# Optimization experiments

Measured on AMD Instinct MI355X. Metric: run time of the kernel, lower is better.

## Reference

```python
import jax, jax.numpy as jnp
import numpy as np

B, T, D = 2, 4096, 512
H = 8
HS = D // H  # 64
CTX = 4096


def setup_inputs() -> dict:
    key = jax.random.key(0)
    ks = jax.random.split(key, 10)
    s = lambda fan_in: fan_in ** -0.5
    x = jax.random.normal(ks[0], (B, T, D), dtype=jnp.float32)
    # per-head q/k/v projections (no bias), stacked over heads: [H, D, HS]
    Wq = jax.random.normal(ks[1], (H, D, HS), dtype=jnp.float32) * s(D)
    Wk = jax.random.normal(ks[2], (H, D, HS), dtype=jnp.float32) * s(D)
    Wv = jax.random.normal(ks[3], (H, D, HS), dtype=jnp.float32) * s(D)
    # output projection [D, D] + bias
    Wproj = jax.random.normal(ks[4], (D, D), dtype=jnp.float32) * s(D)
    bproj = jax.random.normal(ks[5], (D,), dtype=jnp.float32) * 0.01
    # feed-forward: D -> 4D -> D
    W1 = jax.random.normal(ks[6], (D, 4 * D), dtype=jnp.float32) * s(D)
    b1 = jax.random.normal(ks[7], (4 * D,), dtype=jnp.float32) * 0.01
    W2 = jax.random.normal(ks[8], (4 * D, D), dtype=jnp.float32) * s(4 * D)
    b2 = jax.random.normal(ks[9], (D,), dtype=jnp.float32) * 0.01
    return {"x": x, "Wq": Wq, "Wk": Wk, "Wv": Wv, "Wproj": Wproj,
            "bproj": bproj, "W1": W1, "b1": b1, "W2": W2, "b2": b2}


def reference(x, Wq, Wk, Wv, Wproj, bproj, W1, b1, W2, b2):
    Bx, Tx, Dx = x.shape
    scale = HS ** -0.5
    # multi-head causal self-attention (naive, full TxT scores as in source)
    q = jnp.einsum('btd,hde->bhte', x, Wq)
    k = jnp.einsum('btd,hde->bhte', x, Wk)
    v = jnp.einsum('btd,hde->bhte', x, Wv)
    wei = jnp.einsum('bhte,bhse->bhts', q, k) * scale  # [B,H,T,T]
    causal = jnp.tril(jnp.ones((Tx, Tx), dtype=bool))
    wei = jnp.where(causal, wei, -jnp.inf)
    wei = jax.nn.softmax(wei, axis=-1)
    attn = jnp.einsum('bhts,bhse->bhte', wei, v)  # [B,H,T,HS]
    # concat heads (cat along last dim == transpose+reshape of stacked heads)
    attn = attn.transpose(0, 2, 1, 3).reshape(Bx, Tx, Dx)
    sa_out = attn @ Wproj + bproj
    x = x + sa_out
    # feed-forward with residual
    h = jax.nn.relu(x @ W1 + b1)
    x = x + (h @ W2 + b2)
    return x
```

## Files before the change

### kernel.cpp

```cpp
#include <hip/hip_runtime.h>


typedef __attribute__((ext_vector_type(8))) short bf16x8;
typedef __attribute__((ext_vector_type(4))) float f32x4;
typedef __attribute__((ext_vector_type(16))) float f32x16;
typedef unsigned short u16;

__device__ __forceinline__ u16 f2bf(float f) {
  union { float f; unsigned int i; } u; u.f = f;
  unsigned int r = u.i + 0x7fffu + ((u.i >> 16) & 1u);
  return (u16)(r >> 16);
}
__device__ __forceinline__ float bf2f(u16 s) {
  union { unsigned int i; float f; } u; u.i = ((unsigned int)s) << 16;
  return u.f;
}
__device__ __forceinline__ void gload16(const void* g, void* l) {
  __builtin_amdgcn_global_load_lds((const __attribute__((address_space(1))) void*)g,
                                   (__attribute__((address_space(3))) void*)l,
                                   16, 0, 0);
}

__device__ __forceinline__ void plswap_u(unsigned &a, unsigned &b) {
#if defined(__has_builtin) && __has_builtin(__builtin_amdgcn_permlane32_swap)
  auto r = __builtin_amdgcn_permlane32_swap(a, b, false, false);
  a = (unsigned)r[0]; b = (unsigned)r[1];
#else
  asm("v_permlane32_swap_b32 %0, %1" : "+v"(a), "+v"(b));
#endif
}
__device__ __forceinline__ void plswap_f(float &a, float &b) {
  unsigned ua = __builtin_bit_cast(unsigned, a), ub = __builtin_bit_cast(unsigned, b);
  plswap_u(ua, ub);
  a = __builtin_bit_cast(float, ua); b = __builtin_bit_cast(float, ub);
}

__device__ __forceinline__ float tsum16(const f32x16 v) {
  float a = v[0] + v[8],  b = v[1] + v[9];
  float c = v[2] + v[10], d = v[3] + v[11];
  float e = v[4] + v[12], f = v[5] + v[13];
  float g = v[6] + v[14], h = v[7] + v[15];
  a += e; b += f; c += g; d += h;
  a += c; b += d;
  return a + b;
}

__global__ void cast_x_kernel(const float4* __restrict__ in, ushort4* __restrict__ out, int n4) {
  int i = blockIdx.x * blockDim.x + threadIdx.x;
  if (i >= n4) return;
  float4 v = in[i];
  ushort4 o; o.x = f2bf(v.x); o.y = f2bf(v.y); o.z = f2bf(v.z); o.w = f2bf(v.w);
  out[i] = o;
}

__global__ void transpose_cast_kernel(const float* __restrict__ in, u16* __restrict__ out,
                                      int C, int ldo, long in_z, long out_z) {
  __shared__ float t[32][33];
  in += (long)blockIdx.z * in_z;
  out += (long)blockIdx.z * out_z;
  int c0 = blockIdx.x * 32, r0 = blockIdx.y * 32;
  int tx = threadIdx.x & 31, ty = threadIdx.x >> 5;
#pragma unroll
  for (int k = 0; k < 4; k++)
    t[ty + 8 * k][tx] = in[(long)(r0 + ty + 8 * k) * C + c0 + tx];
  __syncthreads();
#pragma unroll
  for (int k = 0; k < 4; k++)
    out[(long)(c0 + ty + 8 * k) * ldo + r0 + tx] = f2bf(t[tx][ty + 8 * k]);
}

__global__ void transpose_v_kernel(const u16* __restrict__ qkv, u16* __restrict__ vt) {
  __shared__ u16 t[32][33];
  int z = blockIdx.z;
  const u16* in = qkv + (long)(z >> 3) * 4096 * 1536 + 1024 + (z & 7) * 64;
  u16* out = vt + (long)z * 64 * 4096;
  int c0 = blockIdx.x * 32, r0 = blockIdx.y * 32;
  int tx = threadIdx.x & 31, ty = threadIdx.x >> 5;
#pragma unroll
  for (int k = 0; k < 4; k++)
    t[ty + 8 * k][tx] = in[(long)(r0 + ty + 8 * k) * 1536 + c0 + tx];
  __syncthreads();
#pragma unroll
  for (int k = 0; k < 4; k++)
    out[(long)(c0 + ty + 8 * k) * 4096 + r0 + tx] = t[tx][ty + 8 * k];
}

template <int MODE, int BN>
__global__ __launch_bounds__(256) void gemm_bt_kernel(
    const u16* __restrict__ A, const u16* __restrict__ Bt, void* __restrict__ Out,
    const float* __restrict__ bias, const float* __restrict__ resf,
    const u16* __restrict__ resb, int N, int K) {
  __shared__ __align__(16) char As[128 * 128];
  __shared__ __align__(16) char Bs[BN * 128];
  const int tid = threadIdx.x;
  const int lane = tid & 63, w = tid >> 6;
  const int l15 = lane & 15, l4 = lane >> 4;
  const int nx = gridDim.x, nwg = nx * gridDim.y;
  int id = blockIdx.y * nx + blockIdx.x;
  id = (id & 7) * (nwg >> 3) + (id >> 3);
  const long m0 = (long)(id / nx) * 128;
  const long n0 = (long)(id % nx) * BN;
  const int wm = (w >> 1) * 64, wn = (w & 1) * (BN / 2);
  const int NB = BN / 32;

  f32x4 acc[4][NB] = {};

  for (int kt = 0; kt < K; kt += 64) {
#pragma unroll
    for (int i = 0; i < 4; i++) {
      int basechunk = i * 256 + w * 64;
      int chunk = basechunk + lane;
      int row = chunk >> 3, c = chunk & 7;
      int sc = c ^ (row & 7);
      gload16(A + (m0 + row) * K + kt + sc * 8, As + basechunk * 16);
    }
#pragma unroll
    for (int i = 0; i < BN / 32; i++) {
      int basechunk = i * 256 + w * 64;
      int chunk = basechunk + lane;
      int row = chunk >> 3, c = chunk & 7;
      int sc = c ^ (row & 7);
      gload16(Bt + (n0 + row) * K + kt + sc * 8, Bs + basechunk * 16);
    }
    __syncthreads();
#pragma unroll
    for (int kk = 0; kk < 2; kk++) {
      bf16x8 a[4], b[NB];
#pragma unroll
      for (int m = 0; m < 4; m++) {
        int row = wm + m * 16 + l15;
        int ch = (kk * 4 + l4) ^ (row & 7);
        a[m] = *(const bf16x8*)(As + row * 128 + ch * 16);
      }
#pragma unroll
      for (int n = 0; n < NB; n++) {
        int row = wn + n * 16 + l15;
        int ch = (kk * 4 + l4) ^ (row & 7);
        b[n] = *(const bf16x8*)(Bs + row * 128 + ch * 16);
      }
#pragma unroll
      for (int m = 0; m < 4; m++)
#pragma unroll
        for (int n = 0; n < NB; n++)
          acc[m][n] = __builtin_amdgcn_mfma_f32_16x16x32_bf16(a[m], b[n], acc[m][n], 0, 0, 0);
    }
    __syncthreads();
  }

#pragma unroll
  for (int m = 0; m < 4; m++) {
#pragma unroll
    for (int n = 0; n < NB; n++) {
      long gcol = n0 + wn + n * 16 + l15;
#pragma unroll
      for (int r = 0; r < 4; r++) {
        long grow = m0 + wm + m * 16 + l4 * 4 + r;
        float v = acc[m][n][r];
        if (MODE == 0) {
          ((u16*)Out)[grow * N + gcol] = f2bf(v);
        } else if (MODE == 1) {
          v += bias[gcol] + resf[grow * N + gcol];
          ((u16*)Out)[grow * N + gcol] = f2bf(v);
        } else if (MODE == 2) {
          v += bias[gcol];
          v = v > 0.f ? v : 0.f;
          ((u16*)Out)[grow * N + gcol] = f2bf(v);
        } else {
          v += bias[gcol] + bf2f(resb[grow * N + gcol]);
          ((float*)Out)[grow * N + gcol] = v;
        }
      }
    }
  }
}

__global__ __launch_bounds__(512, 4) void attn_kernel(
    const u16* __restrict__ qkv, const u16* __restrict__ vt,
    u16* __restrict__ pacc, float* __restrict__ pli) {
  __shared__ __align__(16) char Ks[2][64 * 128];
  __shared__ __align__(16) char Vs[2][64 * 128];
  const int tid = threadIdx.x;
  const int lane = tid & 63, w = tid >> 6;
  const int l31 = lane & 31, l5 = lane >> 5;
  const float cexp = 0.18033688f;

  const int g = blockIdx.x;

  for (int it = 0; it < 2; ++it) {
    const int item = it ? 1023 - g : g;
    const int qt = item >> 6;
    const int bh = (item >> 2) & 15;
    const int qq = item & 3;
    const int b = bh >> 3, h = bh & 7;
    const int qt0 = qt * 256;
    const int L = qt + 1;
    const int j0 = qq * L, j1 = j0 + L;
    const int jdiag = 4 * qt;
    const u16* qbase = qkv + (long)b * 4096 * 1536 + h * 64;
    const u16* kbase = qbase + 512;
    const u16* vtbase = vt + (long)bh * 64 * 4096;

    const int qrow_g = qt0 + w * 32 + l31;
    bf16x8 aq[4];
    {
      const u16* qp = qbase + (long)qrow_g * 1536 + l5 * 8;
#pragma unroll
      for (int kk = 0; kk < 4; kk++) aq[kk] = *(const bf16x8*)(qp + kk * 16);
    }

    {
      int row = tid >> 3, c = tid & 7, sc = c ^ (row & 7);
      gload16(kbase + (long)(j0 * 64 + row) * 1536 + sc * 8, Ks[0] + w * 1024);
      gload16(vtbase + (long)row * 4096 + j0 * 64 + sc * 8, Vs[0] + w * 1024);
    }
    __syncthreads();

    f32x16 oacc[2] = {};
    float li = 0.f;

    for (int j = j0; j < j1; ++j) {
      const int cur = (j - j0) & 1;
      if (j + 1 < j1) {
        int row = tid >> 3, c = tid & 7, sc = c ^ (row & 7);
        gload16(kbase + (long)((j + 1) * 64 + row) * 1536 + sc * 8, Ks[cur ^ 1] + w * 1024);
        gload16(vtbase + (long)row * 4096 + (j + 1) * 64 + sc * 8, Vs[cur ^ 1] + w * 1024);
      }

      const bool diag = (j >= jdiag);
      const int thr = qrow_g - j * 64;

#pragma unroll
      for (int n = 0; n < 2; n++) {
        f32x16 st = {};
        __builtin_amdgcn_s_setprio(1);
#pragma unroll
        for (int kk = 0; kk < 4; kk++) {
          int ch = ((l5 + 2 * kk) ^ (l31 & 7)) * 16;
          bf16x8 ak = *(const bf16x8*)(Ks[cur] + (n * 32 + l31) * 128 + ch);
          st = __builtin_amdgcn_mfma_f32_32x32x16_bf16(ak, aq[kk], st, 0, 0, 0);
        }
        __builtin_amdgcn_s_setprio(0);

        if (diag) {
#pragma unroll
          for (int reg = 0; reg < 16; reg++) {
            int key = n * 32 + 4 * l5 + (reg & 3) + 8 * (reg >> 2);
            if (key > thr) st[reg] = -1e30f;
          }
        }

#pragma unroll
        for (int reg = 0; reg < 16; reg++)
          st[reg] = exp2f(fmaf(st[reg], cexp, -12.f));
        li += tsum16(st);

#pragma unroll
        for (int jj = 0; jj < 2; jj++) {
          unsigned w0, w1, w2, w3;
          {
            unsigned pa, pb;
            asm("v_cvt_pk_bf16_f32 %0, %1, %2" : "=v"(pa) : "v"(st[(2 * jj) * 4 + 0]), "v"(st[(2 * jj) * 4 + 1]));
            asm("v_cvt_pk_bf16_f32 %0, %1, %2" : "=v"(pb) : "v"(st[(2 * jj + 1) * 4 + 0]), "v"(st[(2 * jj + 1) * 4 + 1]));
            plswap_u(pa, pb);
            w0 = pa; w2 = pb;
          }
          {
            unsigned pa, pb;
            asm("v_cvt_pk_bf16_f32 %0, %1, %2" : "=v"(pa) : "v"(st[(2 * jj) * 4 + 2]), "v"(st[(2 * jj) * 4 + 3]));
            asm("v_cvt_pk_bf16_f32 %0, %1, %2" : "=v"(pb) : "v"(st[(2 * jj + 1) * 4 + 2]), "v"(st[(2 * jj + 1) * 4 + 3]));
            plswap_u(pa, pb);
            w1 = pa; w3 = pb;
          }
          union { unsigned u[4]; bf16x8 v; } bp;
          bp.u[0] = w0; bp.u[1] = w1; bp.u[2] = w2; bp.u[3] = w3;
          int s = 2 * n + jj;
          int ch = ((l5 + 2 * s) ^ (l31 & 7)) * 16;
          bf16x8 av0 = *(const bf16x8*)(Vs[cur] + l31 * 128 + ch);
          bf16x8 av1 = *(const bf16x8*)(Vs[cur] + (32 + l31) * 128 + ch);
          __builtin_amdgcn_s_setprio(1);
          oacc[0] = __builtin_amdgcn_mfma_f32_32x32x16_bf16(av0, bp.v, oacc[0], 0, 0, 0);
          oacc[1] = __builtin_amdgcn_mfma_f32_32x32x16_bf16(av1, bp.v, oacc[1], 0, 0, 0);
          __builtin_amdgcn_s_setprio(0);
        }
      }
      __syncthreads();
    }

    {
      float ta = li, tb = li;
      plswap_f(ta, tb);
      li = ta + tb;
    }

    u16* pa = pacc + (long)item * 16384;
#pragma unroll
    for (int ne = 0; ne < 2; ne++)
#pragma unroll
      for (int gg = 0; gg < 4; gg++) {
        ushort4 o;
        o.x = f2bf(oacc[ne][4 * gg + 0]);
        o.y = f2bf(oacc[ne][4 * gg + 1]);
        o.z = f2bf(oacc[ne][4 * gg + 2]);
        o.w = f2bf(oacc[ne][4 * gg + 3]);
        *(ushort4*)(pa + (w * 32 + l31) * 64 + ne * 32 + 4 * l5 + 8 * gg) = o;
      }
    if (l5 == 0) pli[(long)item * 256 + w * 32 + l31] = li;
  }
}

__global__ __launch_bounds__(256) void attn_merge_kernel(
    const u16* __restrict__ pacc, const float* __restrict__ pli, u16* __restrict__ attnb) {
  int tile = blockIdx.x;
  int qt = tile >> 4, bh = tile & 15;
  int b = bh >> 3, h = bh & 7;
  int ibase = qt * 64 + bh * 4;
  const u16* pq[4];
  const float* lq[4];
#pragma unroll
  for (int q = 0; q < 4; q++) {
    pq[q] = pacc + (long)(ibase + q) * 16384;
    lq[q] = pli + (long)(ibase + q) * 256;
  }
  int t = threadIdx.x;
  int cg = (t & 15) * 4;
  int rsub = t >> 4;
#pragma unroll
  for (int pass = 0; pass < 16; ++pass) {
    int row = pass * 16 + rsub;
    float denom = lq[0][row] + lq[1][row] + lq[2][row] + lq[3][row];
    float acc0 = 0.f, acc1 = 0.f, acc2 = 0.f, acc3 = 0.f;
#pragma unroll
    for (int q = 0; q < 4; q++) {
      ushort4 u = *(const ushort4*)(pq[q] + row * 64 + cg);
      acc0 += bf2f(u.x);
      acc1 += bf2f(u.y);
      acc2 += bf2f(u.z);
      acc3 += bf2f(u.w);
    }
    float inv = 1.f / denom;
    ushort4 o;
    o.x = f2bf(acc0 * inv);
    o.y = f2bf(acc1 * inv);
    o.z = f2bf(acc2 * inv);
    o.w = f2bf(acc3 * inv);
    *(ushort4*)(attnb + ((long)(b * 4096 + qt * 256 + row)) * 512 + h * 64 + cg) = o;
  }
}

extern "C" void kernel_launch(void* const* d_in, const int* in_sizes, int n_in,
                              void* d_out, int out_size, void* d_ws, size_t ws_size,
                              hipStream_t stream) {
  const float* x = (const float*)d_in[0];
  const float* Wq = (const float*)d_in[1];
  const float* Wk = (const float*)d_in[2];
  const float* Wv = (const float*)d_in[3];
  const float* Wproj = (const float*)d_in[4];
  const float* bproj = (const float*)d_in[5];
  const float* W1 = (const float*)d_in[6];
  const float* b1 = (const float*)d_in[7];
  const float* W2 = (const float*)d_in[8];
  const float* b2 = (const float*)d_in[9];

  char* ws = (char*)d_ws;
  u16* xb      = (u16*)(ws);
  u16* wqkv_t  = (u16*)(ws + 8388608);
  u16* wproj_t = (u16*)(ws + 9961472);
  u16* w1_t    = (u16*)(ws + 10485760);
  u16* w2_t    = (u16*)(ws + 12582912);
  u16* qkv     = (u16*)(ws + 14680064);
  u16* vt      = (u16*)(ws + 39845888);
  u16* attnb   = (u16*)(ws + 48234496);
  u16* x1b     = (u16*)(ws + 56623104);
  u16* hbuf    = (u16*)(ws + 65011712);
  float* pli   = (float*)(ws + 56623104 + 2097152);
  u16* pacc    = (u16*)(ws + 65011712);

  cast_x_kernel<<<4096, 256, 0, stream>>>((const float4*)x, (ushort4*)xb, 8192 * 512 / 4);

  transpose_cast_kernel<<<dim3(2, 16, 8), 256, 0, stream>>>(Wq, wqkv_t, 64, 512, 32768L, 32768L);
  transpose_cast_kernel<<<dim3(2, 16, 8), 256, 0, stream>>>(Wk, wqkv_t + 512 * 512, 64, 512, 32768L, 32768L);
  transpose_cast_kernel<<<dim3(2, 16, 8), 256, 0, stream>>>(Wv, wqkv_t + 1024 * 512, 64, 512, 32768L, 32768L);
  transpose_cast_kernel<<<dim3(16, 16, 1), 256, 0, stream>>>(Wproj, wproj_t, 512, 512, 0, 0);
  transpose_cast_kernel<<<dim3(64, 16, 1), 256, 0, stream>>>(W1, w1_t, 2048, 512, 0, 0);
  transpose_cast_kernel<<<dim3(16, 64, 1), 256, 0, stream>>>(W2, w2_t, 512, 2048, 0, 0);

  gemm_bt_kernel<0, 128><<<dim3(12, 64), 256, 0, stream>>>(xb, wqkv_t, qkv, nullptr, nullptr, nullptr, 1536, 512);
  transpose_v_kernel<<<dim3(2, 128, 16), 256, 0, stream>>>(qkv, vt);
  attn_kernel<<<512, 512, 0, stream>>>(qkv, vt, pacc, pli);
  attn_merge_kernel<<<256, 256, 0, stream>>>(pacc, pli, attnb);
  gemm_bt_kernel<1, 64><<<dim3(8, 64), 256, 0, stream>>>(attnb, wproj_t, x1b, bproj, x, nullptr, 512, 512);
  gemm_bt_kernel<2, 128><<<dim3(16, 64), 256, 0, stream>>>(x1b, w1_t, hbuf, b1, nullptr, nullptr, 2048, 512);
  gemm_bt_kernel<3, 64><<<dim3(8, 64), 256, 0, stream>>>(hbuf, w2_t, d_out, b2, nullptr, x1b, 512, 2048);
}
```

Measured before the change: 195.8 us.

## Add double-buffered 256x256-tile GEMM kernel for QKV and FFN1 projections

Adds a new 512-thread GEMM kernel with 256x256 output tiles, a 32-wide K step, and double-buffered LDS where the next tile's global-to-LDS loads are interleaved with MFMA work on the current tile. The QKV projection and the first feed-forward GEMM (with bias+ReLU) now use it in place of the 128-wide tile kernel. The aim is more data reuse per tile and overlap of loads with compute. In exchange, far fewer workgroups are launched (192 and 256), which may underfill the GPU's compute units, and register pressure is higher.

```diff
diff --git a/kernel.cpp b/kernel.cpp
--- a/kernel.cpp
+++ b/kernel.cpp
@@ -83,6 +83,100 @@
 #pragma unroll
   for (int k = 0; k < 4; k++)
     out[(long)(c0 + ty + 8 * k) * 4096 + r0 + tx] = t[tx][ty + 8 * k];
+}
+
+template <int MODE>
+__global__ __launch_bounds__(512, 2) void gemm256_kernel(
+    const u16* __restrict__ A, const u16* __restrict__ Bt, void* __restrict__ Out,
+    const float* __restrict__ bias, int N, int K) {
+  __shared__ __align__(16) char As[2][16384];
+  __shared__ __align__(16) char Bs[2][16384];
+  const int tid = threadIdx.x;
+  const int lane = tid & 63, w = tid >> 6;
+  const int l15 = lane & 15, l4 = lane >> 4;
+  const int nx = gridDim.x, nwg = nx * gridDim.y;
+  int id = blockIdx.y * nx + blockIdx.x;
+  id = (id & 7) * (nwg >> 3) + (id >> 3);
+  const long m0 = (long)(id / nx) * 256;
+  const long n0 = (long)(id % nx) * 256;
+  const int wm = (w >> 2) * 128, wn = (w & 3) * 64;
+
+  f32x4 acc[8][4] = {};
+  const int NT = K >> 5;
+
+#pragma unroll
+  for (int i = 0; i < 2; i++) {
+    int basechunk = i * 512 + w * 64;
+    int chunk = basechunk + lane;
+    int row = chunk >> 2, c = chunk & 3;
+    int sc = c ^ ((row >> 1) & 3);
+    gload16(A + (m0 + row) * K + sc * 8, As[0] + basechunk * 16);
+    gload16(Bt + (n0 + row) * K + sc * 8, Bs[0] + basechunk * 16);
+  }
+  __syncthreads();
+
+  for (int t = 0; t < NT; t++) {
+    const int cur = t & 1;
+    const int ktn = (t + 1) << 5;
+    const bool more = (t + 1 < NT);
+#pragma unroll
+    for (int q = 0; q < 4; q++) {
+      if (more) {
+        int i = q & 1;
+        int basechunk = i * 512 + w * 64;
+        int chunk = basechunk + lane;
+        int row = chunk >> 2, c = chunk & 3;
+        int sc = c ^ ((row >> 1) & 3);
+        if (q < 2)
+          gload16(A + (m0 + row) * K + ktn + sc * 8, As[cur ^ 1] + basechunk * 16);
+        else
+          gload16(Bt + (n0 + row) * K + ktn + sc * 8, Bs[cur ^ 1] + basechunk * 16);
+      }
+      const int mh = q >> 1, nh = q & 1;
+      bf16x8 a[4], b[2];
+#pragma unroll
+      for (int i = 0; i < 4; i++) {
+        int row = wm + (mh * 4 + i) * 16 + l15;
+        int ch = l4 ^ ((row >> 1) & 3);
+        a[i] = *(const bf16x8*)(As[cur] + row * 64 + ch * 16);
+      }
+#pragma unroll
+      for (int n = 0; n < 2; n++) {
+        int row = wn + (nh * 2 + n) * 16 + l15;
+        int ch = l4 ^ ((row >> 1) & 3);
+        b[n] = *(const bf16x8*)(Bs[cur] + row * 64 + ch * 16);
+      }
+      __builtin_amdgcn_s_setprio(1);
+#pragma unroll
+      for (int i = 0; i < 4; i++)
+#pragma unroll
+        for (int n = 0; n < 2; n++)
+          acc[mh * 4 + i][nh * 2 + n] = __builtin_amdgcn_mfma_f32_16x16x32_bf16(
+              a[i], b[n], acc[mh * 4 + i][nh * 2 + n], 0, 0, 0);
+      __builtin_amdgcn_s_setprio(0);
+    }
+    __syncthreads();
+  }
+
+#pragma unroll
+  for (int m = 0; m < 8; m++) {
+#pragma unroll
+    for (int n = 0; n < 4; n++) {
+      long gcol = n0 + wn + n * 16 + l15;
+#pragma unroll
+      for (int r = 0; r < 4; r++) {
+        long grow = m0 + wm + m * 16 + l4 * 4 + r;
+        float v = acc[m][n][r];
+        if (MODE == 0) {
+          ((u16*)Out)[grow * N + gcol] = f2bf(v);
+        } else {
+          v += bias[gcol];
+          v = v > 0.f ? v : 0.f;
+          ((u16*)Out)[grow * N + gcol] = f2bf(v);
+        }
+      }
+    }
+  }
 }
 
 template <int MODE, int BN>
@@ -384,11 +478,11 @@
   transpose_cast_kernel<<<dim3(64, 16, 1), 256, 0, stream>>>(W1, w1_t, 2048, 512, 0, 0);
   transpose_cast_kernel<<<dim3(16, 64, 1), 256, 0, stream>>>(W2, w2_t, 512, 2048, 0, 0);
 
-  gemm_bt_kernel<0, 128><<<dim3(12, 64), 256, 0, stream>>>(xb, wqkv_t, qkv, nullptr, nullptr, nullptr, 1536, 512);
+  gemm256_kernel<0><<<dim3(6, 32), 512, 0, stream>>>(xb, wqkv_t, qkv, nullptr, 1536, 512);
   transpose_v_kernel<<<dim3(2, 128, 16), 256, 0, stream>>>(qkv, vt);
   attn_kernel<<<512, 512, 0, stream>>>(qkv, vt, pacc, pli);
   attn_merge_kernel<<<256, 256, 0, stream>>>(pacc, pli, attnb);
   gemm_bt_kernel<1, 64><<<dim3(8, 64), 256, 0, stream>>>(attnb, wproj_t, x1b, bproj, x, nullptr, 512, 512);
-  gemm_bt_kernel<2, 128><<<dim3(16, 64), 256, 0, stream>>>(x1b, w1_t, hbuf, b1, nullptr, nullptr, 2048, 512);
+  gemm256_kernel<2><<<dim3(8, 32), 512, 0, stream>>>(x1b, w1_t, hbuf, b1, 2048, 512);
   gemm_bt_kernel<3, 64><<<dim3(8, 64), 256, 0, stream>>>(hbuf, w2_t, d_out, b2, nullptr, x1b, 512, 2048);
 }
```

Result: slower. 205.3 us (+4.8%).

## Double-buffer GEMM LDS tiles with K=32 steps and MFMA priority

Applied to the files above, without the earlier changes.

Splits the GEMM's LDS tiles into two buffers of half depth (K=32 per step) and prefetches the next K tile with async global-to-LDS loads while the current tile is consumed, using one barrier per iteration. It also raises wave priority around the MFMA block. The aim is to overlap global memory latency with compute. In exchange it doubles the iteration count and barrier frequency and gives less MFMA work per barrier. There is also a risk that the prefetch issued right after the barrier is not waited on before the next iteration reads that buffer.

```diff
diff --git a/kernel.cpp b/kernel.cpp
--- a/kernel.cpp
+++ b/kernel.cpp
@@ -90,8 +90,8 @@
     const u16* __restrict__ A, const u16* __restrict__ Bt, void* __restrict__ Out,
     const float* __restrict__ bias, const float* __restrict__ resf,
     const u16* __restrict__ resb, int N, int K) {
-  __shared__ __align__(16) char As[128 * 128];
-  __shared__ __align__(16) char Bs[BN * 128];
+  __shared__ __align__(16) char As[2][128 * 64];
+  __shared__ __align__(16) char Bs[2][BN * 64];
   const int tid = threadIdx.x;
   const int lane = tid & 63, w = tid >> 6;
   const int l15 = lane & 15, l4 = lane >> 4;
@@ -102,49 +102,65 @@
   const long n0 = (long)(id % nx) * BN;
   const int wm = (w >> 1) * 64, wn = (w & 1) * (BN / 2);
   const int NB = BN / 32;
+  const int NT = K >> 5;
 
   f32x4 acc[4][NB] = {};
 
-  for (int kt = 0; kt < K; kt += 64) {
-#pragma unroll
-    for (int i = 0; i < 4; i++) {
-      int basechunk = i * 256 + w * 64;
-      int chunk = basechunk + lane;
-      int row = chunk >> 3, c = chunk & 7;
-      int sc = c ^ (row & 7);
-      gload16(A + (m0 + row) * K + kt + sc * 8, As + basechunk * 16);
-    }
-#pragma unroll
-    for (int i = 0; i < BN / 32; i++) {
-      int basechunk = i * 256 + w * 64;
-      int chunk = basechunk + lane;
-      int row = chunk >> 3, c = chunk & 7;
-      int sc = c ^ (row & 7);
-      gload16(Bt + (n0 + row) * K + kt + sc * 8, Bs + basechunk * 16);
-    }
+#pragma unroll
+  for (int i = 0; i < 2; i++) {
+    int chunk = i * 256 + tid;
+    int row = chunk >> 2, c = chunk & 3;
+    int sc = c ^ (row & 3);
+    gload16(A + (m0 + row) * K + sc * 8, As[0] + (i * 256 + w * 64) * 16);
+  }
+#pragma unroll
+  for (int i = 0; i < BN / 64; i++) {
+    int chunk = i * 256 + tid;
+    int row = chunk >> 2, c = chunk & 3;
+    int sc = c ^ (row & 3);
+    gload16(Bt + (n0 + row) * K + sc * 8, Bs[0] + (i * 256 + w * 64) * 16);
+  }
+
+  for (int t = 0; t < NT; t++) {
+    const int cur = t & 1;
     __syncthreads();
-#pragma unroll
-    for (int kk = 0; kk < 2; kk++) {
-      bf16x8 a[4], b[NB];
-#pragma unroll
-      for (int m = 0; m < 4; m++) {
-        int row = wm + m * 16 + l15;
-        int ch = (kk * 4 + l4) ^ (row & 7);
-        a[m] = *(const bf16x8*)(As + row * 128 + ch * 16);
-      }
-#pragma unroll
-      for (int n = 0; n < NB; n++) {
-        int row = wn + n * 16 + l15;
-        int ch = (kk * 4 + l4) ^ (row & 7);
-        b[n] = *(const bf16x8*)(Bs + row * 128 + ch * 16);
-      }
-#pragma unroll
-      for (int m = 0; m < 4; m++)
-#pragma unroll
-        for (int n = 0; n < NB; n++)
-          acc[m][n] = __builtin_amdgcn_mfma_f32_16x16x32_bf16(a[m], b[n], acc[m][n], 0, 0, 0);
-    }
-    __syncthreads();
+    if (t + 1 < NT) {
+      const int kt = (t + 1) << 5;
+#pragma unroll
+      for (int i = 0; i < 2; i++) {
+        int chunk = i * 256 + tid;
+        int row = chunk >> 2, c = chunk & 3;
+        int sc = c ^ (row & 3);
+        gload16(A + (m0 + row) * K + kt + sc * 8, As[cur ^ 1] + (i * 256 + w * 64) * 16);
+      }
+#pragma unroll
+      for (int i = 0; i < BN / 64; i++) {
+        int chunk = i * 256 + tid;
+        int row = chunk >> 2, c = chunk & 3;
+        int sc = c ^ (row & 3);
+        gload16(Bt + (n0 + row) * K + kt + sc * 8, Bs[cur ^ 1] + (i * 256 + w * 64) * 16);
+      }
+    }
+    bf16x8 a[4], b[NB];
+#pragma unroll
+    for (int m = 0; m < 4; m++) {
+      int row = wm + m * 16 + l15;
+      int ch = l4 ^ (row & 3);
+      a[m] = *(const bf16x8*)(As[cur] + row * 64 + ch * 16);
+    }
+#pragma unroll
+    for (int n = 0; n < NB; n++) {
+      int row = wn + n * 16 + l15;
+      int ch = l4 ^ (row & 3);
+      b[n] = *(const bf16x8*)(Bs[cur] + row * 64 + ch * 16);
+    }
+    __builtin_amdgcn_s_setprio(1);
+#pragma unroll
+    for (int m = 0; m < 4; m++)
+#pragma unroll
+      for (int n = 0; n < NB; n++)
+        acc[m][n] = __builtin_amdgcn_mfma_f32_16x16x32_bf16(a[m], b[n], acc[m][n], 0, 0, 0);
+    __builtin_amdgcn_s_setprio(0);
   }
 
 #pragma unroll
```

New measurement: 200.5 us. 1.02x slower.
